# Performance work log

Measured on AMD Instinct MI355X. Metric: run time of the kernel, lower is better.

Reference implementation:

```python
import jax, jax.numpy as jnp
import numpy as np

# DeepSeek-V3 MLA attention (q_lora_rank > 0 path), sdpa attn_type (causal)
B, S, DIM = 2, 2048, 2048
NH = 16
Q_LORA = 1536
KV_LORA = 512
NOPE = 128
ROPE = 64
VH = 128
QK_HD = NOPE + ROPE  # 192
EPS = 1e-6
SCALE = QK_HD ** -0.5
ROPE_THETA = 10000.0


def _freqs(seqlen, dim, base):
    f = 1.0 / base ** (np.arange(0, dim, 2, dtype=np.float32) / dim)
    ang = np.outer(np.arange(seqlen, dtype=np.float32), f)
    return jnp.asarray(np.cos(ang)), jnp.asarray(np.sin(ang))


def rmsnorm(x, w, eps=EPS):
    var = jnp.mean(jnp.square(x), axis=-1, keepdims=True)
    return x * jax.lax.rsqrt(var + eps) * w


def apply_rope(x, cos, sin):
    # x: [b, s, h, d]; cos/sin: [s, d//2]; interleaved complex pairs (x[2i], x[2i+1])
    xr, xi = x[..., 0::2], x[..., 1::2]
    c = cos[None, :, None, :]
    s = sin[None, :, None, :]
    yr = xr * c - xi * s
    yi = xr * s + xi * c
    return jnp.stack([yr, yi], axis=-1).reshape(x.shape)


def setup_inputs() -> dict:
    key = jax.random.key(0)
    ks = jax.random.split(key, 7)
    std = 0.02
    x = jax.random.normal(ks[0], (B, S, DIM), dtype=jnp.float32)
    cos, sin = _freqs(S, ROPE, ROPE_THETA)
    return {
        "x": x,
        "freqs_cos": cos,
        "freqs_sin": sin,
        "wq_a": jax.random.normal(ks[1], (DIM, Q_LORA), dtype=jnp.float32) * std,
        "q_norm_w": jnp.ones((Q_LORA,), dtype=jnp.float32),
        "wq_b": jax.random.normal(ks[2], (Q_LORA, NH * QK_HD), dtype=jnp.float32) * std,
        "wkv_a": jax.random.normal(ks[3], (DIM, KV_LORA + ROPE), dtype=jnp.float32) * std,
        "kv_norm_w": jnp.ones((KV_LORA,), dtype=jnp.float32),
        "wkv_b": jax.random.normal(ks[4], (KV_LORA, NH * (NOPE + VH)), dtype=jnp.float32) * std,
        "wo": jax.random.normal(ks[5], (NH * VH, DIM), dtype=jnp.float32) * std,
    }


def reference(x, freqs_cos, freqs_sin, wq_a, q_norm_w, wq_b, wkv_a, kv_norm_w, wkv_b, wo):
    b, s, _ = x.shape
    # low-rank Q projection: wq_a -> RMSNorm -> wq_b
    q = rmsnorm(x @ wq_a, q_norm_w) @ wq_b
    q = q.reshape(b, s, NH, QK_HD)
    q_nope, q_pe = q[..., :NOPE], q[..., NOPE:]
    q_pe = apply_rope(q_pe, freqs_cos, freqs_sin)
    q = jnp.concatenate([q_nope, q_pe], axis=-1)
    # low-rank KV: wkv_a -> split latent / rope part
    kv = x @ wkv_a
    kv_lat, k_pe = kv[..., :KV_LORA], kv[..., KV_LORA:]
    k_pe = apply_rope(k_pe[:, :, None, :], freqs_cos, freqs_sin)  # [b,s,1,ROPE]
    kv = rmsnorm(kv_lat, kv_norm_w) @ wkv_b
    kv = kv.reshape(b, s, NH, NOPE + VH)
    k_nope, v = kv[..., :NOPE], kv[..., NOPE:]
    k = jnp.concatenate([k_nope, jnp.broadcast_to(k_pe, (b, s, NH, ROPE))], axis=-1)
    # attention [b,h,s,d]
    q = q.transpose(0, 2, 1, 3)
    k = k.transpose(0, 2, 1, 3)
    v = v.transpose(0, 2, 1, 3)
    scores = jnp.einsum("bhqd,bhkd->bhqk", q, k) * SCALE
    causal = jnp.tril(jnp.ones((s, s), dtype=bool))
    scores = jnp.where(causal[None, None], scores, jnp.finfo(scores.dtype).min)
    probs = jax.nn.softmax(scores, axis=-1)
    out = jnp.einsum("bhqk,bhkd->bhqd", probs, v)
    out = out.transpose(0, 2, 1, 3).reshape(b, s, NH * VH)
    return out @ wo
```

## Files before the change

### kernel.cpp

```cpp
#include <hip/hip_runtime.h>
#include <cstdint>
#include <cstddef>

typedef __attribute__((ext_vector_type(8))) short bf16x8;
typedef __attribute__((ext_vector_type(4))) float f32x4;
typedef __attribute__((ext_vector_type(16))) float f32x16;

#define S_LEN 2048
#define SCALE2 0.10411754f

__device__ __forceinline__ ushort f2bf(float f) {
  uint32_t u = __float_as_uint(f);
  u = (u + 0x7FFFu + ((u >> 16) & 1u)) >> 16;
  return (ushort)u;
}
__device__ __forceinline__ float bf2f(ushort u) {
  return __uint_as_float(((uint32_t)u) << 16);
}

typedef __attribute__((address_space(1))) void GV;
typedef __attribute__((address_space(3))) void LV;
__device__ __forceinline__ void gload16(const void* g, void* l) {
  __builtin_amdgcn_global_load_lds((GV*)g, (LV*)l, 16, 0, 0);
}

__device__ __forceinline__ void store_out(float* p, float v) { *p = v; }
__device__ __forceinline__ void store_out(ushort* p, float v) { *p = f2bf(v); }

__global__ void k_pre(const float* __restrict__ s0, const float* __restrict__ s1,
                      const float* __restrict__ s2, const float* __restrict__ s3,
                      const float* __restrict__ s4,
                      ushort* __restrict__ d0, ushort* __restrict__ d1,
                      ushort* __restrict__ d2, ushort* __restrict__ d3,
                      ushort* __restrict__ d4,
                      const float* __restrict__ x, ushort* __restrict__ xb) {
  int id = blockIdx.x;
  if (id >= 14976) {
    int ft = threadIdx.y * 32 + threadIdx.x;
    int i = (id - 14976) * 256 + ft;
    const int n4 = 4096 * 2048 / 4, stride = 2048 * 256;
    for (; i < n4; i += stride) {
      float4 v = reinterpret_cast<const float4*>(x)[i];
      ushort4 o;
      o.x = f2bf(v.x); o.y = f2bf(v.y); o.z = f2bf(v.z); o.w = f2bf(v.w);
      reinterpret_cast<ushort4*>(xb)[i] = o;
    }
    return;
  }
  __shared__ float tile[32][33];
  const float* in; ushort* out; int R, C, gx, lid;
  if (id < 3072)        { in = s0; out = d0; R = 2048; C = 1536; gx = 48;  lid = id; }
  else if (id < 4224)   { in = s1; out = d1; R = 2048; C = 576;  gx = 18;  lid = id - 3072; }
  else if (id < 8832)   { in = s2; out = d2; R = 1536; C = 3072; gx = 96;  lid = id - 4224; }
  else if (id < 10880)  { in = s3; out = d3; R = 512;  C = 4096; gx = 128; lid = id - 8832; }
  else                  { in = s4; out = d4; R = 2048; C = 2048; gx = 64;  lid = id - 10880; }
  int c0 = (lid % gx) * 32, r0 = (lid / gx) * 32;
  int tx = threadIdx.x, ty = threadIdx.y;
#pragma unroll
  for (int i = 0; i < 32; i += 8) {
    int r = r0 + ty + i, c = c0 + tx;
    if (r < R && c < C) tile[ty + i][tx] = in[(size_t)r * C + c];
  }
  __syncthreads();
#pragma unroll
  for (int i = 0; i < 32; i += 8) {
    int c = c0 + ty + i, r = r0 + tx;
    if (r < R && c < C) out[(size_t)c * R + r] = f2bf(tile[tx][ty + i]);
  }
}

template <typename OUT>
__global__ __launch_bounds__(256) void k_gemm(const ushort* __restrict__ A,
                                              const ushort* __restrict__ Bt,
                                              OUT* __restrict__ C, int K, int Nreal) {
  __shared__ ushort As[128 * 72];
  __shared__ ushort Bs[128 * 72];
  const int t = threadIdx.x, lane = t & 63, w = t >> 6;
  const int nwg = gridDim.x * gridDim.y;
  const int wg = blockIdx.y * gridDim.x + blockIdx.x;
  const int swz = (wg & 7) * (nwg >> 3) + (wg >> 3);
  const int m0 = (swz / gridDim.x) * 128, n0 = (swz % gridDim.x) * 128;
  const int wm = (w >> 1) * 64, wn = (w & 1) * 64;
  const int g = lane >> 4, q = lane & 15;
  f32x4 acc[4][4] = {};
  for (int kt = 0; kt < K; kt += 64) {
#pragma unroll
    for (int it = 0; it < 5; ++it) {
      int ii = it * 4 + w;
      if (ii < 18) {
        unsigned s = ii * 64 + lane;
        int r = s / 9, e = s - r * 9;
        int cg = e ^ ((r >> 3) & 7);
        if (cg > 7) cg = 0;
        gload16(A + (size_t)(m0 + r) * K + kt + cg * 8, (char*)As + ii * 1024);
        gload16(Bt + (size_t)(n0 + r) * K + kt + cg * 8, (char*)Bs + ii * 1024);
      }
    }
    asm volatile("s_waitcnt vmcnt(0)" ::: "memory");
    __syncthreads();
#pragma unroll
    for (int kh = 0; kh < 2; ++kh) {
      bf16x8 af[4], bfr[4];
#pragma unroll
      for (int mi = 0; mi < 4; mi++) {
        int row = wm + 16 * mi + q;
        int rx = (row >> 3) & 7;
        af[mi] = *(const bf16x8*)(As + row * 72 + (((kh * 4 + g) ^ rx) << 3));
      }
#pragma unroll
      for (int ni = 0; ni < 4; ni++) {
        int row = wn + 16 * ni + q;
        int rx = (row >> 3) & 7;
        bfr[ni] = *(const bf16x8*)(Bs + row * 72 + (((kh * 4 + g) ^ rx) << 3));
      }
#pragma unroll
      for (int mi = 0; mi < 4; mi++)
#pragma unroll
        for (int ni = 0; ni < 4; ni++)
          acc[mi][ni] = __builtin_amdgcn_mfma_f32_16x16x32_bf16(af[mi], bfr[ni], acc[mi][ni], 0, 0, 0);
    }
    __syncthreads();
  }
#pragma unroll
  for (int mi = 0; mi < 4; mi++)
#pragma unroll
    for (int ni = 0; ni < 4; ni++) {
      int col = n0 + wn + 16 * ni + q;
      if (col < Nreal) {
        int row = m0 + wm + 16 * mi + 4 * g;
#pragma unroll
        for (int r = 0; r < 4; r++)
          store_out(&C[(size_t)(row + r) * Nreal + col], acc[mi][ni][r]);
      }
    }
}

__global__ __launch_bounds__(256) void k_gemm_qkv(const ushort* __restrict__ A1,
                                                  const ushort* __restrict__ Bt1,
                                                  ushort* __restrict__ C1,
                                                  const float* __restrict__ cosT,
                                                  const float* __restrict__ sinT,
                                                  const ushort* __restrict__ A2,
                                                  const ushort* __restrict__ Bt2,
                                                  ushort* __restrict__ kbuf,
                                                  ushort* __restrict__ vT) {
  __shared__ ushort As[128 * 72];
  __shared__ ushort Bs[128 * 72];
  const int t = threadIdx.x, lane = t & 63, w = t >> 6;
  const int wm = (w >> 1) * 64, wn = (w & 1) * 64;
  const int g = lane >> 4, q = lane & 15;
  const int id = blockIdx.x;

  if (id < 768) {
    const int K = 1536, gx = 24, nwg = 768;
    const int wg = id;
    const int swz = (wg & 7) * (nwg >> 3) + (wg >> 3);
    const int m0 = (swz / gx) * 128, n0 = (swz % gx) * 128;
    f32x4 acc[4][4] = {};
    for (int kt = 0; kt < K; kt += 64) {
#pragma unroll
      for (int it = 0; it < 5; ++it) {
        int ii = it * 4 + w;
        if (ii < 18) {
          unsigned s = ii * 64 + lane;
          int r = s / 9, e = s - r * 9;
          int cg = e ^ ((r >> 3) & 7);
          if (cg > 7) cg = 0;
          gload16(A1 + (size_t)(m0 + r) * K + kt + cg * 8, (char*)As + ii * 1024);
          gload16(Bt1 + (size_t)(n0 + r) * K + kt + cg * 8, (char*)Bs + ii * 1024);
        }
      }
      asm volatile("s_waitcnt vmcnt(0)" ::: "memory");
      __syncthreads();
#pragma unroll
      for (int kh = 0; kh < 2; ++kh) {
        bf16x8 af[4], bfr[4];
#pragma unroll
        for (int mi = 0; mi < 4; mi++) {
          int row = wm + 16 * mi + q;
          int rx = (row >> 3) & 7;
          af[mi] = *(const bf16x8*)(As + row * 72 + (((kh * 4 + g) ^ rx) << 3));
        }
#pragma unroll
        for (int ni = 0; ni < 4; ni++) {
          int row = wn + 16 * ni + q;
          int rx = (row >> 3) & 7;
          bfr[ni] = *(const bf16x8*)(Bs + row * 72 + (((kh * 4 + g) ^ rx) << 3));
        }
#pragma unroll
        for (int mi = 0; mi < 4; mi++)
#pragma unroll
          for (int ni = 0; ni < 4; ni++)
            acc[mi][ni] = __builtin_amdgcn_mfma_f32_16x16x32_bf16(af[mi], bfr[ni], acc[mi][ni], 0, 0, 0);
      }
      __syncthreads();
    }
#pragma unroll
    for (int mi = 0; mi < 4; mi++)
#pragma unroll
      for (int ni = 0; ni < 4; ni++) {
        int col = n0 + wn + 16 * ni + q;
        int hoff = col % 192;
        int row = m0 + wm + 16 * mi + 4 * g;
        if (hoff < 128) {
#pragma unroll
          for (int r = 0; r < 4; r++)
            C1[(size_t)(row + r) * 3072 + col] = f2bf(acc[mi][ni][r]);
        } else {
          int i = (hoff - 128) >> 1;
#pragma unroll
          for (int r = 0; r < 4; r++) {
            int s2 = (row + r) & 2047;
            float c = cosT[s2 * 32 + i], sn = sinT[s2 * 32 + i];
            float v = acc[mi][ni][r];
            float p = __shfl_xor(v, 1);
            float res = (q & 1) ? (p * sn + v * c) : (v * c - p * sn);
            C1[(size_t)(row + r) * 3072 + col] = f2bf(res);
          }
        }
      }
  } else {
    const int K = 512, gx = 32, nwg = 1024;
    const int wg = id - 768;
    const int swz = (wg & 7) * (nwg >> 3) + (wg >> 3);
    const int m0 = (swz / gx) * 128, n0 = (swz % gx) * 128;
    f32x4 acc[4][4] = {};
    for (int kt = 0; kt < K; kt += 64) {
#pragma unroll
      for (int it = 0; it < 5; ++it) {
        int ii = it * 4 + w;
        if (ii < 18) {
          unsigned s = ii * 64 + lane;
          int r = s / 9, e = s - r * 9;
          int cg = e ^ ((r >> 3) & 7);
          if (cg > 7) cg = 0;
          gload16(A2 + (size_t)(m0 + r) * K + kt + cg * 8, (char*)As + ii * 1024);
          gload16(Bt2 + (size_t)(n0 + r) * K + kt + cg * 8, (char*)Bs + ii * 1024);
        }
      }
      asm volatile("s_waitcnt vmcnt(0)" ::: "memory");
      __syncthreads();
#pragma unroll
      for (int kh = 0; kh < 2; ++kh) {
        bf16x8 af[4], bfr[4];
#pragma unroll
        for (int mi = 0; mi < 4; mi++) {
          int row = wm + 16 * mi + q;
          int rx = (row >> 3) & 7;
          af[mi] = *(const bf16x8*)(As + row * 72 + (((kh * 4 + g) ^ rx) << 3));
        }
#pragma unroll
        for (int ni = 0; ni < 4; ni++) {
          int row = wn + 16 * ni + q;
          int rx = (row >> 3) & 7;
          bfr[ni] = *(const bf16x8*)(Bs + row * 72 + (((kh * 4 + g) ^ rx) << 3));
        }
#pragma unroll
        for (int mi = 0; mi < 4; mi++)
#pragma unroll
          for (int ni = 0; ni < 4; ni++)
            acc[mi][ni] = __builtin_amdgcn_mfma_f32_16x16x32_bf16(af[mi], bfr[ni], acc[mi][ni], 0, 0, 0);
      }
      __syncthreads();
    }
#pragma unroll
    for (int mi = 0; mi < 4; mi++)
#pragma unroll
      for (int ni = 0; ni < 4; ni++) {
        int col = n0 + wn + 16 * ni + q;
        int hh = col >> 8, jj = col & 255;
        int row0 = m0 + wm + 16 * mi + 4 * g;
#pragma unroll
        for (int r = 0; r < 4; r++) {
          int tok = row0 + r;
          int bb = tok >> 11, ss = tok & 2047;
          ushort v = f2bf(acc[mi][ni][r]);
          if (jj < 128)
            kbuf[((size_t)(bb * 16 + hh) * 2048 + ss) * 192 + jj] = v;
          else
            vT[((size_t)(bb * 16 + hh) * 128 + (jj - 128)) * 2048 + ss] = v;
        }
      }
  }
}

__global__ void k_norms(const ushort* __restrict__ cqkv, const float* __restrict__ qnw,
                        const float* __restrict__ kvnw,
                        const float* __restrict__ cosT, const float* __restrict__ sinT,
                        ushort* __restrict__ cqn, ushort* __restrict__ ckvn,
                        ushort* __restrict__ kbuf) {
  __shared__ float red[4];
  int id = blockIdx.x;
  if (id < 4096) {
    int row = id;
    const ushort* x = cqkv + (size_t)row * 2112;
    ushort* o = cqn + (size_t)row * 1536;
    float ss = 0.f;
    for (int i = threadIdx.x; i < 1536; i += 256) { float v = bf2f(x[i]); ss += v * v; }
#pragma unroll
    for (int m = 1; m < 64; m <<= 1) ss += __shfl_xor(ss, m);
    if ((threadIdx.x & 63) == 0) red[threadIdx.x >> 6] = ss;
    __syncthreads();
    float tot = red[0] + red[1] + red[2] + red[3];
    float sc = rsqrtf(tot / 1536.f + 1e-6f);
    for (int i = threadIdx.x; i < 1536; i += 256) o[i] = f2bf(bf2f(x[i]) * sc * qnw[i]);
  } else {
    int tok = id - 4096, b = tok >> 11, s = tok & 2047;
    const ushort* x = cqkv + (size_t)tok * 2112 + 1536;
    float ss = 0.f;
    for (int i = threadIdx.x; i < 512; i += 256) { float v = bf2f(x[i]); ss += v * v; }
#pragma unroll
    for (int m = 1; m < 64; m <<= 1) ss += __shfl_xor(ss, m);
    if ((threadIdx.x & 63) == 0) red[threadIdx.x >> 6] = ss;
    __syncthreads();
    float tot = red[0] + red[1] + red[2] + red[3];
    float sc = rsqrtf(tot / 512.f + 1e-6f);
    for (int i = threadIdx.x; i < 512; i += 256) ckvn[(size_t)tok * 512 + i] = f2bf(bf2f(x[i]) * sc * kvnw[i]);
    if (threadIdx.x < 32) {
      int i = threadIdx.x;
      float xr = bf2f(x[512 + 2 * i]), xi = bf2f(x[512 + 2 * i + 1]);
      float c = cosT[s * 32 + i], sn = sinT[s * 32 + i];
      uint32_t lo = f2bf(xr * c - xi * sn);
      uint32_t hi = f2bf(xr * sn + xi * c);
      uint32_t pk = lo | (hi << 16);
#pragma unroll
      for (int h = 0; h < 16; ++h)
        *(uint32_t*)(kbuf + ((size_t)(b * 16 + h) * 2048 + s) * 192 + 128 + 2 * i) = pk;
    }
  }
}

__global__ __launch_bounds__(256, 2) void k_attn10(const ushort* __restrict__ qb,
                                                   const ushort* __restrict__ kb,
                                                   const ushort* __restrict__ vT,
                                                   ushort* __restrict__ aout) {
  const int id = blockIdx.x;
  const int qt = (id < 256) ? (15 - (id >> 5)) : ((id - 256) >> 5);
  const int bh = id & 31;
  const int h = bh & 15, b = bh >> 4;

  const int t = threadIdx.x, lane = t & 63, w = t >> 6;
  const int lq = lane & 31, hi = lane >> 5;
  const int kx = (lq >> 3) & 3;

  __shared__ ushort Ks[64 * 200];
  __shared__ ushort Vs[128 * 72];

  const ushort* kh = kb + (size_t)(b * 16 + h) * (2048 * 192);
  const ushort* vh = vT + (size_t)(b * 16 + h) * (128 * 2048);

  auto stage = [&](int k0) {
#pragma unroll
    for (int it = 0; it < 7; ++it) {
      int ii = it * 4 + w;
      if (ii < 25) {
        unsigned s = ii * 64 + lane;
        int r = s / 25, e = s - r * 25;
        int cg = e ^ ((r >> 3) & 3);
        if (cg > 23) cg = 0;
        gload16(kh + (size_t)(k0 + r) * 192 + cg * 8, (char*)Ks + ii * 1024);
      }
    }
#pragma unroll
    for (int it = 0; it < 5; ++it) {
      int ii = it * 4 + w;
      if (ii < 18) {
        unsigned s = ii * 64 + lane;
        int r = s / 9, e = s - r * 9;
        int cg = e ^ ((r >> 3) & 7);
        if (cg > 7) cg = 0;
        gload16(vh + (size_t)r * 2048 + k0 + cg * 8, (char*)Vs + ii * 1024);
      }
    }
  };

  const int q0 = qt * 128;
  const int q0w = q0 + 32 * w;
  const int qg = q0w + lq;
  const int nkt = qt * 2 + 2;

  bf16x8 qf[12];
  {
    const ushort* qp = qb + ((size_t)(b * 2048 + qg) * 16 + h) * 192 + 8 * hi;
#pragma unroll
    for (int s = 0; s < 12; ++s) qf[s] = *(const bf16x8*)(qp + 16 * s);
  }

  f32x16 oacc[4];
#pragma unroll
  for (int db = 0; db < 4; ++db)
#pragma unroll
    for (int r = 0; r < 16; ++r) oacc[db][r] = 0.f;
  float m = -1e30f, l = 0.f;

  for (int kt = 0; kt < nkt; ++kt) {
    const int k0 = kt * 64;
    stage(k0);
    asm volatile("s_waitcnt vmcnt(0)" ::: "memory");
    __syncthreads();
    if (k0 <= q0w + 31) {
      f32x16 sA, sB;
#pragma unroll
      for (int r = 0; r < 16; ++r) { sA[r] = 0.f; sB[r] = 0.f; }
      __builtin_amdgcn_s_setprio(1);
#pragma unroll
      for (int s = 0; s < 12; ++s) {
        int ch = ((2 * s + hi) ^ kx) << 3;
        bf16x8 kfA = *(const bf16x8*)(Ks + lq * 200 + ch);
        bf16x8 kfB = *(const bf16x8*)(Ks + (lq + 32) * 200 + ch);
        sA = __builtin_amdgcn_mfma_f32_32x32x16_bf16(kfA, qf[s], sA, 0, 0, 0);
        sB = __builtin_amdgcn_mfma_f32_32x32x16_bf16(kfB, qf[s], sB, 0, 0, 0);
      }
      __builtin_amdgcn_s_setprio(0);
      float svA[16], svB[16];
#pragma unroll
      for (int r = 0; r < 16; ++r) { svA[r] = sA[r]; svB[r] = sB[r]; }
      if (k0 + 63 > q0w) {
#pragma unroll
        for (int r = 0; r < 16; ++r) {
          int kk = (r & 3) + 8 * (r >> 2) + 4 * hi;
          if (k0 + kk > qg) svA[r] = -1e30f;
          if (k0 + 32 + kk > qg) svB[r] = -1e30f;
        }
      }
      float pmax = fmaxf(svA[0], svB[0]);
#pragma unroll
      for (int r = 1; r < 16; ++r) pmax = fmaxf(pmax, fmaxf(svA[r], svB[r]));
      pmax = fmaxf(pmax, __shfl_xor(pmax, 32));
      float smax = pmax * SCALE2;
      if (!__all(smax - m <= 8.0f)) {
        float mnew = fmaxf(m, smax);
        float a = exp2f(m - mnew);
        l *= a;
#pragma unroll
        for (int db = 0; db < 4; ++db)
#pragma unroll
          for (int r = 0; r < 16; ++r) oacc[db][r] *= a;
        m = mnew;
      }
      float eA[16], eB[16]; float sum = 0.f;
#pragma unroll
      for (int r = 0; r < 16; ++r) {
        eA[r] = exp2f(svA[r] * SCALE2 - m);
        eB[r] = exp2f(svB[r] * SCALE2 - m);
        sum += eA[r] + eB[r];
      }
      sum += __shfl_xor(sum, 32);
      l += sum;
      uint32_t pkA[8], pkB[8];
#pragma unroll
      for (int i = 0; i < 8; ++i) {
        pkA[i] = (uint32_t)f2bf(eA[2 * i]) | ((uint32_t)f2bf(eA[2 * i + 1]) << 16);
        pkB[i] = (uint32_t)f2bf(eB[2 * i]) | ((uint32_t)f2bf(eB[2 * i + 1]) << 16);
      }
      uint32_t swA[8], swB[8];
#pragma unroll
      for (int i = 0; i < 8; ++i) {
        swA[i] = (uint32_t)__shfl_xor((int)pkA[i], 32);
        swB[i] = (uint32_t)__shfl_xor((int)pkB[i], 32);
      }
      union { uint32_t u[4]; bf16x8 v; } pA0, pA1, pB0, pB1;
      pA0.u[0] = hi ? swA[2] : pkA[0];
      pA0.u[1] = hi ? swA[3] : pkA[1];
      pA0.u[2] = hi ? pkA[2] : swA[0];
      pA0.u[3] = hi ? pkA[3] : swA[1];
      pA1.u[0] = hi ? swA[6] : pkA[4];
      pA1.u[1] = hi ? swA[7] : pkA[5];
      pA1.u[2] = hi ? pkA[6] : swA[4];
      pA1.u[3] = hi ? pkA[7] : swA[5];
      pB0.u[0] = hi ? swB[2] : pkB[0];
      pB0.u[1] = hi ? swB[3] : pkB[1];
      pB0.u[2] = hi ? pkB[2] : swB[0];
      pB0.u[3] = hi ? pkB[3] : swB[1];
      pB1.u[0] = hi ? swB[6] : pkB[4];
      pB1.u[1] = hi ? swB[7] : pkB[5];
      pB1.u[2] = hi ? pkB[6] : swB[4];
      pB1.u[3] = hi ? pkB[7] : swB[5];
      __builtin_amdgcn_s_setprio(1);
#pragma unroll
      for (int db = 0; db < 4; ++db) {
        const int d = 32 * db + lq;
        const int vx = (d >> 3) & 7;
        const ushort* vr = Vs + d * 72;
        bf16x8 vf0 = *(const bf16x8*)(vr + (((0 + hi) ^ vx) << 3));
        bf16x8 vf1 = *(const bf16x8*)(vr + (((2 + hi) ^ vx) << 3));
        bf16x8 vf2 = *(const bf16x8*)(vr + (((4 + hi) ^ vx) << 3));
        bf16x8 vf3 = *(const bf16x8*)(vr + (((6 + hi) ^ vx) << 3));
        oacc[db] = __builtin_amdgcn_mfma_f32_32x32x16_bf16(vf0, pA0.v, oacc[db], 0, 0, 0);
        oacc[db] = __builtin_amdgcn_mfma_f32_32x32x16_bf16(vf1, pA1.v, oacc[db], 0, 0, 0);
        oacc[db] = __builtin_amdgcn_mfma_f32_32x32x16_bf16(vf2, pB0.v, oacc[db], 0, 0, 0);
        oacc[db] = __builtin_amdgcn_mfma_f32_32x32x16_bf16(vf3, pB1.v, oacc[db], 0, 0, 0);
      }
      __builtin_amdgcn_s_setprio(0);
    }
    asm volatile("s_waitcnt lgkmcnt(0)" ::: "memory");
    __syncthreads();
  }

  float inv = 1.f / l;
  ushort* op = aout + ((size_t)(b * 2048 + qg)) * 2048 + h * 128 + 4 * hi;
#pragma unroll
  for (int db = 0; db < 4; ++db)
#pragma unroll
    for (int i = 0; i < 8; ++i) {
      uint32_t u = (uint32_t)f2bf(oacc[db][2 * i] * inv) |
                   ((uint32_t)f2bf(oacc[db][2 * i + 1] * inv) << 16);
      int dbase = 32 * db + (i & 1) * 2 + (i >> 1) * 8;
      *(uint32_t*)(op + dbase) = u;
    }
}

extern "C" void kernel_launch(void* const* d_in, const int* in_sizes, int n_in,
                              void* d_out, int out_size, void* d_ws, size_t ws_size,
                              hipStream_t stream) {
  const float* x = (const float*)d_in[0];
  const float* fcos = (const float*)d_in[1];
  const float* fsin = (const float*)d_in[2];
  const float* wq_a = (const float*)d_in[3];
  const float* qnw = (const float*)d_in[4];
  const float* wq_b = (const float*)d_in[5];
  const float* wkv_a = (const float*)d_in[6];
  const float* kvnw = (const float*)d_in[7];
  const float* wkv_b = (const float*)d_in[8];
  const float* wo = (const float*)d_in[9];
  float* out = (float*)d_out;

  char* ws = (char*)d_ws;
  size_t off = 0;
  auto alloc = [&](size_t bytes) -> char* {
    char* p = ws + off;
    off += (bytes + 255) & ~(size_t)255;
    return p;
  };
  ushort* xb     = (ushort*)alloc(4096ull * 2048 * 2);
  ushort* wqkv_t = (ushort*)alloc(2176ull * 2048 * 2);
  ushort* wqb_t  = (ushort*)alloc(3072ull * 1536 * 2);
  ushort* wkvb_t = (ushort*)alloc(4096ull * 512 * 2);
  ushort* wo_t   = (ushort*)alloc(2048ull * 2048 * 2);
  ushort* cqkv   = (ushort*)alloc(4096ull * 2112 * 2);
  ushort* cqn    = (ushort*)alloc(4096ull * 1536 * 2);
  ushort* ckvn   = (ushort*)alloc(4096ull * 512 * 2);
  ushort* kbuf   = (ushort*)alloc(2ull * 16 * 2048 * 192 * 2);
  ushort* qbuf   = (ushort*)alloc(4096ull * 3072 * 2);
  ushort* aout   = xb;
  ushort* vT     = cqkv;

  k_pre<<<17024, dim3(32, 8), 0, stream>>>(
      wq_a, wkv_a, wq_b, wkv_b, wo,
      wqkv_t, wqkv_t + 1536ull * 2048, wqb_t, wkvb_t, wo_t,
      x, xb);

  k_gemm<ushort><<<dim3(17, 32), 256, 0, stream>>>(xb, wqkv_t, cqkv, 2048, 2112);

  k_norms<<<8192, 256, 0, stream>>>(cqkv, qnw, kvnw, fcos, fsin, cqn, ckvn, kbuf);

  k_gemm_qkv<<<1792, 256, 0, stream>>>(cqn, wqb_t, qbuf, fcos, fsin,
                                       ckvn, wkvb_t, kbuf, vT);

  k_attn10<<<dim3(512), 256, 0, stream>>>(qbuf, kbuf, vT, aout);

  k_gemm<float><<<dim3(16, 32), 256, 0, stream>>>(aout, wo_t, out, 2048, 2048);
}
```

Baseline: 336.5 us.

## Rewrite fused QKV GEMM with 256x256 tiles, 8 waves, double-buffered LDS

Replaces the 128x128-tile fused Q/KV up-projection GEMM with a 256x256-tile version using 512 threads (8 waves, each computing 128x64), a double-buffered LDS pipeline that prefetches two K-steps ahead with partial vmcnt waits, and s_setprio around the MFMA block. Larger tiles raise arithmetic intensity and cut global traffic. The prefetch is meant to overlap loads with compute instead of the previous load-wait-compute serialization. In exchange it launches only 448 workgroups at one workgroup per CU, uses about 147KB of LDS, and drops the XOR swizzle in favour of 144-byte row padding, which may change LDS bank-conflict behaviour.

```diff
diff --git a/kernel.cpp b/kernel.cpp
--- a/kernel.cpp
+++ b/kernel.cpp
@@ -135,73 +135,90 @@
     }
 }
 
-__global__ __launch_bounds__(256) void k_gemm_qkv(const ushort* __restrict__ A1,
-                                                  const ushort* __restrict__ Bt1,
-                                                  ushort* __restrict__ C1,
-                                                  const float* __restrict__ cosT,
-                                                  const float* __restrict__ sinT,
-                                                  const ushort* __restrict__ A2,
-                                                  const ushort* __restrict__ Bt2,
-                                                  ushort* __restrict__ kbuf,
-                                                  ushort* __restrict__ vT) {
-  __shared__ ushort As[128 * 72];
-  __shared__ ushort Bs[128 * 72];
+__global__ __launch_bounds__(512, 1) void k_gemm_qkv256(
+    const ushort* __restrict__ A1, const ushort* __restrict__ Bt1,
+    ushort* __restrict__ C1,
+    const float* __restrict__ cosT, const float* __restrict__ sinT,
+    const ushort* __restrict__ A2, const ushort* __restrict__ Bt2,
+    ushort* __restrict__ kbuf, ushort* __restrict__ vT) {
+  __shared__ __align__(16) char lds[2][4][18432];
   const int t = threadIdx.x, lane = t & 63, w = t >> 6;
-  const int wm = (w >> 1) * 64, wn = (w & 1) * 64;
-  const int g = lane >> 4, q = lane & 15;
+  const int q = lane & 15, g = lane >> 4;
+  const int wm = w >> 2, wn = w & 3;
   const int id = blockIdx.x;
-
-  if (id < 768) {
-    const int K = 1536, gx = 24, nwg = 768;
-    const int wg = id;
-    const int swz = (wg & 7) * (nwg >> 3) + (wg >> 3);
-    const int m0 = (swz / gx) * 128, n0 = (swz % gx) * 128;
-    f32x4 acc[4][4] = {};
-    for (int kt = 0; kt < K; kt += 64) {
-#pragma unroll
-      for (int it = 0; it < 5; ++it) {
-        int ii = it * 4 + w;
-        if (ii < 18) {
-          unsigned s = ii * 64 + lane;
-          int r = s / 9, e = s - r * 9;
-          int cg = e ^ ((r >> 3) & 7);
-          if (cg > 7) cg = 0;
-          gload16(A1 + (size_t)(m0 + r) * K + kt + cg * 8, (char*)As + ii * 1024);
-          gload16(Bt1 + (size_t)(n0 + r) * K + kt + cg * 8, (char*)Bs + ii * 1024);
-        }
-      }
-      asm volatile("s_waitcnt vmcnt(0)" ::: "memory");
-      __syncthreads();
-#pragma unroll
-      for (int kh = 0; kh < 2; ++kh) {
-        bf16x8 af[4], bfr[4];
-#pragma unroll
-        for (int mi = 0; mi < 4; mi++) {
-          int row = wm + 16 * mi + q;
-          int rx = (row >> 3) & 7;
-          af[mi] = *(const bf16x8*)(As + row * 72 + (((kh * 4 + g) ^ rx) << 3));
-        }
-#pragma unroll
-        for (int ni = 0; ni < 4; ni++) {
-          int row = wn + 16 * ni + q;
-          int rx = (row >> 3) & 7;
-          bfr[ni] = *(const bf16x8*)(Bs + row * 72 + (((kh * 4 + g) ^ rx) << 3));
-        }
-#pragma unroll
-        for (int mi = 0; mi < 4; mi++)
-#pragma unroll
-          for (int ni = 0; ni < 4; ni++)
-            acc[mi][ni] = __builtin_amdgcn_mfma_f32_16x16x32_bf16(af[mi], bfr[ni], acc[mi][ni], 0, 0, 0);
-      }
-      __syncthreads();
-    }
-#pragma unroll
-    for (int mi = 0; mi < 4; mi++)
-#pragma unroll
-      for (int ni = 0; ni < 4; ni++) {
-        int col = n0 + wn + 16 * ni + q;
+  const bool seg1 = (id < 192);
+  const ushort* A  = seg1 ? A1 : A2;
+  const ushort* Bt = seg1 ? Bt1 : Bt2;
+  const int K   = seg1 ? 1536 : 512;
+  const int gx  = seg1 ? 12 : 16;
+  const int nwg = seg1 ? 192 : 256;
+  const int wg  = seg1 ? id : id - 192;
+  const int swz = (wg & 7) * (nwg >> 3) + (wg >> 3);
+  const int m0 = (swz / gx) * 256, n0 = (swz % gx) * 256;
+  const int nt = K >> 6;
+
+  auto stageTile = [&](int kt, int p) {
+#pragma unroll
+    for (int it = 0; it < 9; ++it) {
+      int u = it * 512 + (w << 6);
+      int hh = u / 1152;
+      int s0 = u - hh * 1152;
+      int s = s0 + lane;
+      int r = s / 9, c = s - r * 9;
+      if (c > 7) c = 0;
+      const ushort* src = (hh < 2) ? (A + (size_t)(m0 + (hh << 7) + r) * K)
+                                   : (Bt + (size_t)(n0 + ((hh - 2) << 7) + r) * K);
+      gload16(src + kt * 64 + c * 8, &lds[p][hh][s0 * 16]);
+    }
+  };
+
+  f32x4 acc[8][4] = {};
+  stageTile(0, 0);
+  asm volatile("" ::: "memory");
+  stageTile(1, 1);
+
+  for (int kt = 0; kt < nt; ++kt) {
+    const int p = kt & 1;
+    if (kt == 0 || kt + 1 >= nt) asm volatile("s_waitcnt vmcnt(0)" ::: "memory");
+    else                         asm volatile("s_waitcnt vmcnt(9)" ::: "memory");
+    __builtin_amdgcn_s_barrier();
+    asm volatile("" ::: "memory");
+    const char* LA = &lds[p][wm][0];
+    const char* LB = &lds[p][2 + (wn >> 1)][0];
+    const int brow0 = (wn & 1) * 64;
+    bf16x8 bfr[4][2];
+#pragma unroll
+    for (int ni = 0; ni < 4; ++ni) {
+      bfr[ni][0] = *(const bf16x8*)(LB + (brow0 + ni * 16 + q) * 144 + 16 * g);
+      bfr[ni][1] = *(const bf16x8*)(LB + (brow0 + ni * 16 + q) * 144 + 64 + 16 * g);
+    }
+    __builtin_amdgcn_s_setprio(1);
+#pragma unroll
+    for (int mi = 0; mi < 8; ++mi) {
+      bf16x8 a0 = *(const bf16x8*)(LA + (mi * 16 + q) * 144 + 16 * g);
+      bf16x8 a1 = *(const bf16x8*)(LA + (mi * 16 + q) * 144 + 64 + 16 * g);
+#pragma unroll
+      for (int ni = 0; ni < 4; ++ni)
+        acc[mi][ni] = __builtin_amdgcn_mfma_f32_16x16x32_bf16(a0, bfr[ni][0], acc[mi][ni], 0, 0, 0);
+#pragma unroll
+      for (int ni = 0; ni < 4; ++ni)
+        acc[mi][ni] = __builtin_amdgcn_mfma_f32_16x16x32_bf16(a1, bfr[ni][1], acc[mi][ni], 0, 0, 0);
+    }
+    __builtin_amdgcn_s_setprio(0);
+    asm volatile("s_waitcnt lgkmcnt(0)" ::: "memory");
+    __builtin_amdgcn_s_barrier();
+    asm volatile("" ::: "memory");
+    if (kt + 2 < nt) stageTile(kt + 2, p);
+  }
+
+  if (seg1) {
+#pragma unroll
+    for (int mi = 0; mi < 8; ++mi)
+#pragma unroll
+      for (int ni = 0; ni < 4; ++ni) {
+        int col = n0 + wn * 64 + ni * 16 + q;
         int hoff = col % 192;
-        int row = m0 + wm + 16 * mi + 4 * g;
+        int row = m0 + wm * 128 + mi * 16 + 4 * g;
         if (hoff < 128) {
 #pragma unroll
           for (int r = 0; r < 4; r++)
@@ -213,63 +230,20 @@
             int s2 = (row + r) & 2047;
             float c = cosT[s2 * 32 + i], sn = sinT[s2 * 32 + i];
             float v = acc[mi][ni][r];
-            float p = __shfl_xor(v, 1);
-            float res = (q & 1) ? (p * sn + v * c) : (v * c - p * sn);
+            float pv = __shfl_xor(v, 1);
+            float res = (q & 1) ? (pv * sn + v * c) : (v * c - pv * sn);
             C1[(size_t)(row + r) * 3072 + col] = f2bf(res);
           }
         }
       }
   } else {
-    const int K = 512, gx = 32, nwg = 1024;
-    const int wg = id - 768;
-    const int swz = (wg & 7) * (nwg >> 3) + (wg >> 3);
-    const int m0 = (swz / gx) * 128, n0 = (swz % gx) * 128;
-    f32x4 acc[4][4] = {};
-    for (int kt = 0; kt < K; kt += 64) {
-#pragma unroll
-      for (int it = 0; it < 5; ++it) {
-        int ii = it * 4 + w;
-        if (ii < 18) {
-          unsigned s = ii * 64 + lane;
-          int r = s / 9, e = s - r * 9;
-          int cg = e ^ ((r >> 3) & 7);
-          if (cg > 7) cg = 0;
-          gload16(A2 + (size_t)(m0 + r) * K + kt + cg * 8, (char*)As + ii * 1024);
-          gload16(Bt2 + (size_t)(n0 + r) * K + kt + cg * 8, (char*)Bs + ii * 1024);
-        }
-      }
-      asm volatile("s_waitcnt vmcnt(0)" ::: "memory");
-      __syncthreads();
-#pragma unroll
-      for (int kh = 0; kh < 2; ++kh) {
-        bf16x8 af[4], bfr[4];
-#pragma unroll
-        for (int mi = 0; mi < 4; mi++) {
-          int row = wm + 16 * mi + q;
-          int rx = (row >> 3) & 7;
-          af[mi] = *(const bf16x8*)(As + row * 72 + (((kh * 4 + g) ^ rx) << 3));
-        }
-#pragma unroll
-        for (int ni = 0; ni < 4; ni++) {
-          int row = wn + 16 * ni + q;
-          int rx = (row >> 3) & 7;
-          bfr[ni] = *(const bf16x8*)(Bs + row * 72 + (((kh * 4 + g) ^ rx) << 3));
-        }
-#pragma unroll
-        for (int mi = 0; mi < 4; mi++)
-#pragma unroll
-          for (int ni = 0; ni < 4; ni++)
-            acc[mi][ni] = __builtin_amdgcn_mfma_f32_16x16x32_bf16(af[mi], bfr[ni], acc[mi][ni], 0, 0, 0);
-      }
-      __syncthreads();
-    }
-#pragma unroll
-    for (int mi = 0; mi < 4; mi++)
-#pragma unroll
-      for (int ni = 0; ni < 4; ni++) {
-        int col = n0 + wn + 16 * ni + q;
+#pragma unroll
+    for (int mi = 0; mi < 8; ++mi)
+#pragma unroll
+      for (int ni = 0; ni < 4; ++ni) {
+        int col = n0 + wn * 64 + ni * 16 + q;
         int hh = col >> 8, jj = col & 255;
-        int row0 = m0 + wm + 16 * mi + 4 * g;
+        int row0 = m0 + wm * 128 + mi * 16 + 4 * g;
 #pragma unroll
         for (int r = 0; r < 4; r++) {
           int tok = row0 + r;
@@ -554,8 +528,8 @@
 
   k_norms<<<8192, 256, 0, stream>>>(cqkv, qnw, kvnw, fcos, fsin, cqn, ckvn, kbuf);
 
-  k_gemm_qkv<<<1792, 256, 0, stream>>>(cqn, wqb_t, qbuf, fcos, fsin,
-                                       ckvn, wkvb_t, kbuf, vT);
+  k_gemm_qkv256<<<448, 512, 0, stream>>>(cqn, wqb_t, qbuf, fcos, fsin,
+                                         ckvn, wkvb_t, kbuf, vT);
 
   k_attn10<<<dim3(512), 256, 0, stream>>>(qbuf, kbuf, vT, aout);
 
```

Result: faster. 329.5 us, median of 2 (-2.1%).
